# Kernel optimization log

Hardware: AMD Instinct MI355X
Metric: run time of the kernel (lower is better)

Reference implementation:

```python
import jax, jax.numpy as jnp
import numpy as np

NEG_SLOPE = 0.2  # PyG GATv2Conv default negative_slope


def gatv2(x, edge_index, w_l, w_r, att, bias):
    # x: [G, N, F]  (G = batch*step independent graphs sharing edge_index)
    G, N, F = x.shape
    H, C = att.shape
    # add self loops (PyG default add_self_loops=True)
    loops = jnp.arange(N, dtype=edge_index.dtype)
    src = jnp.concatenate([edge_index[0], loops])  # [E]
    dst = jnp.concatenate([edge_index[1], loops])  # [E]
    # linear projections for source / target nodes
    x_l = (x @ w_l).reshape(G, N, H, C)  # source projection
    x_r = (x @ w_r).reshape(G, N, H, C)  # target projection
    # gather along edges -> [E, G, H, C] (edge axis leading for segment ops)
    src_f = jnp.take(x_l, src, axis=1).transpose(1, 0, 2, 3)
    dst_f = jnp.take(x_r, dst, axis=1).transpose(1, 0, 2, 3)
    # GATv2 attention logit: a^T leaky_relu(W_l x_j + W_r x_i)
    e = jax.nn.leaky_relu(src_f + dst_f, NEG_SLOPE)
    logit = jnp.einsum('eghc,hc->egh', e, att)  # [E, G, H]
    # numerically-stable segment softmax over incoming edges per dst node
    m = jax.ops.segment_max(logit, dst, num_segments=N)  # [N, G, H]
    ex = jnp.exp(logit - m[dst])
    denom = jax.ops.segment_sum(ex, dst, num_segments=N)  # [N, G, H]
    alpha = ex / denom[dst]  # [E, G, H]
    # weighted scatter-add aggregation
    out = jax.ops.segment_sum(alpha[..., None] * src_f, dst, num_segments=N)  # [N,G,H,C]
    out = out.transpose(1, 0, 2, 3).reshape(G, N, H * C) + bias
    return out


def setup_inputs() -> dict:
    key = jax.random.key(0)
    ks = jax.random.split(key, 6)
    B, T, N, F = 8, 10, 1000, 64
    E, H, C = 8000, 1, 64
    x = jax.random.normal(ks[0], (B, T, N, F), dtype=jnp.float32)
    edge_index = jax.random.randint(ks[1], (2, E), 0, N, dtype=jnp.int64)
    s = 1.0 / np.sqrt(F)
    w_l = jax.random.normal(ks[2], (F, H * C), dtype=jnp.float32) * s
    w_r = jax.random.normal(ks[3], (F, H * C), dtype=jnp.float32) * s
    att = jax.random.normal(ks[4], (H, C), dtype=jnp.float32) * (1.0 / np.sqrt(C))
    bias = jnp.zeros((H * C,), dtype=jnp.float32)
    return {"x": x, "edge_index": edge_index, "w_l": w_l, "w_r": w_r, "att": att, "bias": bias}


def reference(x, edge_index, w_l, w_r, att, bias):
    B, T, N, F = x.shape
    out = gatv2(x.reshape(B * T, N, F), edge_index, w_l, w_r, att, bias)
    return out.reshape(B, T, N, -1)
```

## Files before the change

### kernel.cpp

```cpp
#include <hip/hip_runtime.h>
#include <hip/hip_bf16.h>


#define GG 80
#define NN 1000
#define EE 8000
#define MM 80000
#define NEG_SLOPE 0.2f

typedef __attribute__((ext_vector_type(8))) short short8;
typedef __attribute__((ext_vector_type(4))) float floatx4;

__device__ __forceinline__ unsigned short f2b(float f) {
    unsigned int u = __float_as_uint(f);
    unsigned int r = u + 0x7fffu + ((u >> 16) & 1u);
    return (unsigned short)(r >> 16);
}

__global__ __launch_bounds__(256) void proj_kernel(
    const float* __restrict__ x,
    const float* __restrict__ wl,
    const float* __restrict__ wr,
    unsigned short* __restrict__ XLt,
    unsigned short* __restrict__ XRt)
{
    __shared__ __align__(16) unsigned short Wt[128 * 72];
    const int t = threadIdx.x;

    for (int idx = t; idx < 8192; idx += 256) {
        int half = idx >> 12;
        int k = (idx & 4095) >> 6;
        int c = idx & 63;
        float v = half ? wr[k * 64 + c] : wl[k * 64 + c];
        Wt[(c + half * 64) * 72 + k] = f2b(v);
    }
    __syncthreads();

    const int wave = t >> 6;
    const int lane = t & 63;
    const int quad = lane >> 4;
    const int lm   = lane & 15;
    const int Rb   = (blockIdx.x * 4 + wave) * 64;

    short8 Bf[2][8];
#pragma unroll
    for (int ks = 0; ks < 2; ks++)
#pragma unroll
        for (int sub = 0; sub < 8; sub++)
            Bf[ks][sub] = *(const short8*)(&Wt[(sub * 16 + lm) * 72 + ks * 32 + quad * 8]);

    const float4* x4 = (const float4*)x;

#pragma unroll
    for (int sm = 0; sm < 4; sm++) {
        const int rbase = Rb + sm * 16;
        const int r  = rbase + lm;
        const int rc = (r < MM) ? r : (MM - 1);

        short8 Af[2];
#pragma unroll
        for (int ks = 0; ks < 2; ks++) {
            float4 p = x4[(size_t)rc * 16 + ks * 8 + quad * 2];
            float4 q = x4[(size_t)rc * 16 + ks * 8 + quad * 2 + 1];
            short8 a;
            a[0] = (short)f2b(p.x); a[1] = (short)f2b(p.y);
            a[2] = (short)f2b(p.z); a[3] = (short)f2b(p.w);
            a[4] = (short)f2b(q.x); a[5] = (short)f2b(q.y);
            a[6] = (short)f2b(q.z); a[7] = (short)f2b(q.w);
            Af[ks] = a;
        }

        floatx4 acc[8];
#pragma unroll
        for (int sub = 0; sub < 8; sub++) acc[sub] = (floatx4)(0.f);
#pragma unroll
        for (int ks = 0; ks < 2; ks++)
#pragma unroll
            for (int sub = 0; sub < 8; sub++)
                acc[sub] = __builtin_amdgcn_mfma_f32_16x16x32_bf16(Af[ks], Bf[ks][sub], acc[sub], 0, 0, 0);

#pragma unroll
        for (int reg = 0; reg < 4; reg++) {
            int rr = rbase + quad * 4 + reg;
            if (rr < MM) {
                int g = rr / 1000;
                int n = rr - g * 1000;
                size_t ob = ((size_t)n * GG + g) * 64 + lm;
#pragma unroll
                for (int sub = 0; sub < 4; sub++)
                    XLt[ob + sub * 16] = f2b(acc[sub][reg]);
#pragma unroll
                for (int sub = 4; sub < 8; sub++)
                    XRt[ob + (sub - 4) * 16] = f2b(acc[sub][reg]);
            }
        }
    }
}

__global__ __launch_bounds__(640) void agg_kernel(
    const unsigned short* __restrict__ XLt,
    const unsigned short* __restrict__ XRt,
    const int* __restrict__ ei32,
    const float* __restrict__ att,
    const float* __restrict__ bias,
    float* __restrict__ out)
{
    __shared__ int elist[1024];
    __shared__ int s_cnt;
    __shared__ int s_odd;
    const int t = threadIdx.x;
    const int d = blockIdx.x;
    const int g = t >> 3;
    const int cg = t & 7;

    if (t == 0) { s_cnt = 0; s_odd = 0; }
    __syncthreads();
    for (int e = t; e < 2048; e += 640)
        if (ei32[2 * e + 1] != 0) s_odd = 1;
    __syncthreads();
    const int stride = s_odd ? 1 : 2;

    for (int e = t; e < EE; e += 640) {
        int de = ei32[(size_t)(EE + e) * stride];
        if (de == d) {
            int p = atomicAdd(&s_cnt, 1);
            if (p < 1023) elist[p] = ei32[(size_t)e * stride];
        }
    }
    __syncthreads();
    if (t == 0) { elist[min(s_cnt, 1023)] = d; s_cnt = min(s_cnt, 1023) + 1; }
    __syncthreads();
    const int cnt = s_cnt;

    float xr[8], av[8];
    {
        const uint4 u = *(const uint4*)(XRt + ((size_t)d * GG + g) * 64 + cg * 8);
        const unsigned int uw[4] = {u.x, u.y, u.z, u.w};
#pragma unroll
        for (int q = 0; q < 4; q++) {
            xr[2 * q + 0] = __uint_as_float(uw[q] << 16);
            xr[2 * q + 1] = __uint_as_float(uw[q] & 0xffff0000u);
        }
#pragma unroll
        for (int j = 0; j < 8; j++) av[j] = att[cg * 8 + j];
    }

    float acc[8];
#pragma unroll
    for (int j = 0; j < 8; j++) acc[j] = 0.f;
    float dn = 0.f;

    for (int i = 0; i < cnt; i++) {
        int s = elist[i];
        const uint4 u = *(const uint4*)(XLt + ((size_t)s * GG + g) * 64 + cg * 8);
        const unsigned int uw[4] = {u.x, u.y, u.z, u.w};
        float xf[8];
#pragma unroll
        for (int q = 0; q < 4; q++) {
            xf[2 * q + 0] = __uint_as_float(uw[q] << 16);
            xf[2 * q + 1] = __uint_as_float(uw[q] & 0xffff0000u);
        }
        float p = 0.f;
#pragma unroll
        for (int j = 0; j < 8; j++) {
            float v = xf[j] + xr[j];
            float lv = fmaxf(v, 0.f) + NEG_SLOPE * fminf(v, 0.f);
            p = fmaf(av[j], lv, p);
        }
        p += __shfl_xor(p, 1, 64);
        p += __shfl_xor(p, 2, 64);
        p += __shfl_xor(p, 4, 64);
        float w = __expf(p);
        dn += w;
#pragma unroll
        for (int j = 0; j < 8; j++) acc[j] = fmaf(w, xf[j], acc[j]);
    }

    const float inv = 1.f / dn;
    float4 r0, r1;
    r0.x = acc[0] * inv + bias[cg * 8 + 0];
    r0.y = acc[1] * inv + bias[cg * 8 + 1];
    r0.z = acc[2] * inv + bias[cg * 8 + 2];
    r0.w = acc[3] * inv + bias[cg * 8 + 3];
    r1.x = acc[4] * inv + bias[cg * 8 + 4];
    r1.y = acc[5] * inv + bias[cg * 8 + 5];
    r1.z = acc[6] * inv + bias[cg * 8 + 6];
    r1.w = acc[7] * inv + bias[cg * 8 + 7];
    float* po = out + ((size_t)g * NN + d) * 64 + cg * 8;
    *(float4*)po = r0;
    *(float4*)(po + 4) = r1;
}

extern "C" void kernel_launch(void* const* d_in, const int* in_sizes, int n_in,
                              void* d_out, int out_size, void* d_ws, size_t ws_size,
                              hipStream_t stream) {
    const float* x    = (const float*)d_in[0];
    const int*   ei   = (const int*)d_in[1];
    const float* wl   = (const float*)d_in[2];
    const float* wr   = (const float*)d_in[3];
    const float* att  = (const float*)d_in[4];
    const float* bias = (const float*)d_in[5];
    float* out = (float*)d_out;

    char* ws = (char*)d_ws;
    unsigned short* XLt = (unsigned short*)ws;
    unsigned short* XRt = XLt + (size_t)NN * GG * 64;

    hipLaunchKernelGGL(proj_kernel, dim3((MM + 255) / 256), dim3(256), 0, stream,
                       x, wl, wr, XLt, XRt);
    hipLaunchKernelGGL(agg_kernel, dim3(NN), dim3(640), 0, stream,
                       XLt, XRt, ei, att, bias, out);
}
```

Before: 121.0 us.

## Split aggregation across two graph-halves, unroll edge loop by three, hoist loads

The aggregation kernel now launches a 2D grid with 320-thread blocks, each covering half of the 80 graphs, instead of one 640-thread block per destination node. The edge loop is unrolled by three so three independent gathers from XLt are in flight at once. The XRt, att and bias loads are hoisted ahead of the edge-list build so their latency overlaps it. In exchange, every block now rescans the full edge list, doubling that scan work, and the per-node edge list is capped at 255 entries instead of 1023.

After: 129.4 us. 7.0% more time.

```diff
diff --git a/kernel.cpp b/kernel.cpp
--- a/kernel.cpp
+++ b/kernel.cpp
@@ -97,7 +97,7 @@
     }
 }
 
-__global__ __launch_bounds__(640) void agg_kernel(
+__global__ __launch_bounds__(320) void agg_kernel(
     const unsigned short* __restrict__ XLt,
     const unsigned short* __restrict__ XRt,
     const int* __restrict__ ei32,
@@ -105,59 +105,97 @@
     const float* __restrict__ bias,
     float* __restrict__ out)
 {
-    __shared__ int elist[1024];
+    __shared__ int elist[256];
     __shared__ int s_cnt;
     __shared__ int s_odd;
     const int t = threadIdx.x;
     const int d = blockIdx.x;
-    const int g = t >> 3;
+    const int g = blockIdx.y * 40 + (t >> 3);
     const int cg = t & 7;
 
     if (t == 0) { s_cnt = 0; s_odd = 0; }
-    __syncthreads();
-    for (int e = t; e < 2048; e += 640)
+
+    float xr[8], av[8], bv[8];
+    {
+        const uint4 u = *(const uint4*)(XRt + ((size_t)d * GG + g) * 64 + cg * 8);
+        const unsigned int uw[4] = {u.x, u.y, u.z, u.w};
+#pragma unroll
+        for (int q = 0; q < 4; q++) {
+            xr[2 * q + 0] = __uint_as_float(uw[q] << 16);
+            xr[2 * q + 1] = __uint_as_float(uw[q] & 0xffff0000u);
+        }
+#pragma unroll
+        for (int j = 0; j < 8; j++) { av[j] = att[cg * 8 + j]; bv[j] = bias[cg * 8 + j]; }
+    }
+
+    __syncthreads();
+    for (int e = t; e < 2048; e += 320)
         if (ei32[2 * e + 1] != 0) s_odd = 1;
     __syncthreads();
     const int stride = s_odd ? 1 : 2;
 
-    for (int e = t; e < EE; e += 640) {
+    for (int e = t; e < EE; e += 320) {
         int de = ei32[(size_t)(EE + e) * stride];
         if (de == d) {
             int p = atomicAdd(&s_cnt, 1);
-            if (p < 1023) elist[p] = ei32[(size_t)e * stride];
-        }
-    }
-    __syncthreads();
-    if (t == 0) { elist[min(s_cnt, 1023)] = d; s_cnt = min(s_cnt, 1023) + 1; }
+            if (p < 255) elist[p] = ei32[(size_t)e * stride];
+        }
+    }
+    __syncthreads();
+    if (t == 0) { int c = min(s_cnt, 255); elist[c] = d; s_cnt = c + 1; }
     __syncthreads();
     const int cnt = s_cnt;
-
-    float xr[8], av[8];
-    {
-        const uint4 u = *(const uint4*)(XRt + ((size_t)d * GG + g) * 64 + cg * 8);
-        const unsigned int uw[4] = {u.x, u.y, u.z, u.w};
-#pragma unroll
-        for (int q = 0; q < 4; q++) {
-            xr[2 * q + 0] = __uint_as_float(uw[q] << 16);
-            xr[2 * q + 1] = __uint_as_float(uw[q] & 0xffff0000u);
-        }
-#pragma unroll
-        for (int j = 0; j < 8; j++) av[j] = att[cg * 8 + j];
-    }
 
     float acc[8];
 #pragma unroll
     for (int j = 0; j < 8; j++) acc[j] = 0.f;
     float dn = 0.f;
 
-    for (int i = 0; i < cnt; i++) {
+    int i = 0;
+    for (; i + 3 <= cnt; i += 3) {
+        int s0 = elist[i], s1 = elist[i + 1], s2 = elist[i + 2];
+        uint4 u0 = *(const uint4*)(XLt + ((size_t)s0 * GG + g) * 64 + cg * 8);
+        uint4 u1 = *(const uint4*)(XLt + ((size_t)s1 * GG + g) * 64 + cg * 8);
+        uint4 u2 = *(const uint4*)(XLt + ((size_t)s2 * GG + g) * 64 + cg * 8);
+        float xf[3][8];
+        {
+            const unsigned int w0[4] = {u0.x, u0.y, u0.z, u0.w};
+            const unsigned int w1[4] = {u1.x, u1.y, u1.z, u1.w};
+            const unsigned int w2[4] = {u2.x, u2.y, u2.z, u2.w};
+#pragma unroll
+            for (int q = 0; q < 4; q++) {
+                xf[0][2 * q] = __uint_as_float(w0[q] << 16); xf[0][2 * q + 1] = __uint_as_float(w0[q] & 0xffff0000u);
+                xf[1][2 * q] = __uint_as_float(w1[q] << 16); xf[1][2 * q + 1] = __uint_as_float(w1[q] & 0xffff0000u);
+                xf[2][2 * q] = __uint_as_float(w2[q] << 16); xf[2][2 * q + 1] = __uint_as_float(w2[q] & 0xffff0000u);
+            }
+        }
+        float p[3] = {0.f, 0.f, 0.f};
+#pragma unroll
+        for (int e = 0; e < 3; e++)
+#pragma unroll
+            for (int j = 0; j < 8; j++) {
+                float v = xf[e][j] + xr[j];
+                float lv = fmaxf(v, 0.f) + NEG_SLOPE * fminf(v, 0.f);
+                p[e] = fmaf(av[j], lv, p[e]);
+            }
+#pragma unroll
+        for (int m = 1; m <= 4; m <<= 1)
+#pragma unroll
+            for (int e = 0; e < 3; e++) p[e] += __shfl_xor(p[e], m, 64);
+        float w0 = __expf(p[0]), w1 = __expf(p[1]), w2 = __expf(p[2]);
+        dn += w0 + w1 + w2;
+#pragma unroll
+        for (int j = 0; j < 8; j++)
+            acc[j] = fmaf(w2, xf[2][j], fmaf(w1, xf[1][j], fmaf(w0, xf[0][j], acc[j])));
+    }
+    for (; i < cnt; i++) {
         int s = elist[i];
         const uint4 u = *(const uint4*)(XLt + ((size_t)s * GG + g) * 64 + cg * 8);
         const unsigned int uw[4] = {u.x, u.y, u.z, u.w};
         float xf[8];
 #pragma unroll
         for (int q = 0; q < 4; q++) {
-            xf[2 * q + 0] = __uint_as_float(uw[q] << 16);
+            xf[2 * q] = __uint_as_float(uw[q] << 16);
             xf[2 * q + 1] = __uint_as_float(uw[q] & 0xffff0000u);
         }
         float p = 0.f;
@@ -178,14 +216,14 @@
 
     const float inv = 1.f / dn;
     float4 r0, r1;
-    r0.x = acc[0] * inv + bias[cg * 8 + 0];
-    r0.y = acc[1] * inv + bias[cg * 8 + 1];
-    r0.z = acc[2] * inv + bias[cg * 8 + 2];
-    r0.w = acc[3] * inv + bias[cg * 8 + 3];
-    r1.x = acc[4] * inv + bias[cg * 8 + 4];
-    r1.y = acc[5] * inv + bias[cg * 8 + 5];
-    r1.z = acc[6] * inv + bias[cg * 8 + 6];
-    r1.w = acc[7] * inv + bias[cg * 8 + 7];
+    r0.x = acc[0] * inv + bv[0];
+    r0.y = acc[1] * inv + bv[1];
+    r0.z = acc[2] * inv + bv[2];
+    r0.w = acc[3] * inv + bv[3];
+    r1.x = acc[4] * inv + bv[4];
+    r1.y = acc[5] * inv + bv[5];
+    r1.z = acc[6] * inv + bv[6];
+    r1.w = acc[7] * inv + bv[7];
     float* po = out + ((size_t)g * NN + d) * 64 + cg * 8;
     *(float4*)po = r0;
     *(float4*)(po + 4) = r1;
@@ -208,6 +246,6 @@
 
     hipLaunchKernelGGL(proj_kernel, dim3((MM + 255) / 256), dim3(256), 0, stream,
                        x, wl, wr, XLt, XRt);
-    hipLaunchKernelGGL(agg_kernel, dim3(NN), dim3(640), 0, stream,
+    hipLaunchKernelGGL(agg_kernel, dim3(NN, 2), dim3(320), 0, stream,
                        XLt, XRt, ei, att, bias, out);
 }
```
